# Performance work log

Hardware: AMD Instinct MI355X
Metric: run time of the kernel (lower is better)

## Reference

```python
import jax, jax.numpy as jnp
import numpy as np

N = 8192
NEG = -1e9  # masked-logit fill (finite to stay fp16/bf16-safe)


def _gat_layer(x, W, a_src, a_dst, adj, apply_elu):
    # x: [N, Fin], W: [Fin, Fout]
    h = x @ W                                   # [N, Fout]
    f_src = h @ a_src                           # [N] attention contribution of source i
    f_dst = h @ a_dst                           # [N] attention contribution of target j
    e = jax.nn.leaky_relu(f_src[:, None] + f_dst[None, :], negative_slope=0.2)  # [N, N]
    e = jnp.where(adj > 0, e, NEG)
    attn = jax.nn.softmax(e, axis=1)            # masked neighbor softmax per node
    out = attn @ h                              # [N, Fout]
    return jax.nn.elu(out) if apply_elu else out


def setup_inputs() -> dict:
    key = jax.random.key(0)
    ks = jax.random.split(key, 8)
    x = jax.random.normal(ks[0], (N, 512), dtype=jnp.float32)
    E_rand = 262144
    ei = jax.random.randint(ks[1], (2, E_rand), 0, N, dtype=jnp.int64)
    loops = jnp.broadcast_to(jnp.arange(N, dtype=jnp.int64), (2, N))
    edge_index = jnp.concatenate([ei, loops], axis=1)  # self-loops avoid empty softmax rows
    W1 = jax.random.normal(ks[2], (512, 256), dtype=jnp.float32) * (1.0 / np.sqrt(512))
    a1_src = jax.random.normal(ks[3], (256,), dtype=jnp.float32) * 0.1
    a1_dst = jax.random.normal(ks[4], (256,), dtype=jnp.float32) * 0.1
    W2 = jax.random.normal(ks[5], (256, 16), dtype=jnp.float32) * (1.0 / np.sqrt(256))
    a2_src = jax.random.normal(ks[6], (16,), dtype=jnp.float32) * 0.1
    a2_dst = jax.random.normal(ks[7], (16,), dtype=jnp.float32) * 0.1
    return {"x": x, "edge_index": edge_index, "W1": W1, "a1_src": a1_src,
            "a1_dst": a1_dst, "W2": W2, "a2_src": a2_src, "a2_dst": a2_dst}


def reference(x, edge_index, W1, a1_src, a1_dst, W2, a2_src, a2_dst):
    # dense adjacency scatter, exactly as the torch module does
    adj = jnp.zeros((N, N), dtype=x.dtype).at[edge_index[0], edge_index[1]].set(1.0)
    # inference: dropout disabled
    h = _gat_layer(x, W1, a1_src, a1_dst, adj, apply_elu=True)
    logits = _gat_layer(h, W2, a2_src, a2_dst, adj, apply_elu=False)
    return jax.nn.log_softmax(logits, axis=1)
```

## Files before the change

kernel.cpp:

```cpp
#include <hip/hip_runtime.h>
#include <hip/hip_bf16.h>


#define NN 8192
#define MAXD 128

typedef __bf16 bf16x8 __attribute__((ext_vector_type(8)));
typedef float f32x4 __attribute__((ext_vector_type(4)));
typedef unsigned short u16x8 __attribute__((ext_vector_type(8)));

__device__ __forceinline__ unsigned short f2bf(float f) {
  unsigned u = __float_as_uint(f);
  unsigned r = (u + 0x7fffu + ((u >> 16) & 1u)) >> 16;
  return (unsigned short)r;
}
__device__ __forceinline__ float bf2f(unsigned short u) {
  return __uint_as_float(((unsigned)u) << 16);
}
__device__ __forceinline__ float lrelu02(float e) { return e > 0.f ? e : 0.2f * e; }

__global__ __launch_bounds__(256) void prep_kernel(uint4* __restrict__ bitmap,
                                                   const float* __restrict__ W1,
                                                   unsigned short* __restrict__ W1t,
                                                   const float* __restrict__ W2,
                                                   unsigned short* __restrict__ W2t,
                                                   float4* __restrict__ f1sd) {
  const int bid = blockIdx.x, tid = threadIdx.x;
  if (bid < 2048) {
    bitmap[bid * 256 + tid] = uint4{0u, 0u, 0u, 0u};
  } else if (bid < 2560) {
    const int gid = (bid - 2048) * 256 + tid;
    const int n = gid >> 9, k = gid & 511;
    W1t[gid] = f2bf(W1[(size_t)k * 256 + n]);
  } else if (bid == 2560) {
    for (int i = tid; i < 16 * 256; i += 256) {
      const int n = i >> 8, k = i & 255;
      W2t[i] = f2bf(W2[(size_t)k * 16 + n]);
    }
  } else {
    for (int i = tid; i < 4096; i += 256) f1sd[i] = float4{0.f, 0.f, 0.f, 0.f};
  }
}

__global__ void scatter_kernel(const int* __restrict__ ei, int E,
                               unsigned* __restrict__ bitmap) {
  const int t = blockIdx.x * 256 + threadIdx.x;
  if (t >= E) return;
  const int s = ei[t];
  const int d = ei[E + t];
  atomicOr(bitmap + (size_t)s * 256 + (d >> 5), 1u << (d & 31));
}

__global__ __launch_bounds__(256) void gemm1_mfma_kernel(
    const float* __restrict__ X, const unsigned short* __restrict__ W1t,
    unsigned short* __restrict__ h1b, const float* __restrict__ A1S,
    const float* __restrict__ A1D, float* __restrict__ f1s, float* __restrict__ f1d) {
  constexpr int K = 512;
  __shared__ __align__(16) unsigned short lds[1024 * 8];
  const int t = threadIdx.x;
  const int w = t >> 6, l = t & 63;
  const int lr = l & 15, lg = l >> 4;
  const int bm = blockIdx.x * 64, bn = blockIdx.y * 64;
  const int r8 = t >> 3, c8 = t & 7;

  f32x4 acc[4];
  const f32x4 fz = {0.f, 0.f, 0.f, 0.f};
#pragma unroll
  for (int cb = 0; cb < 4; ++cb) acc[cb] = fz;

  for (int k0 = 0; k0 < K; k0 += 64) {
    float4 xa[2][2];
#pragma unroll
    for (int p = 0; p < 2; ++p) {
      const float* s = X + (size_t)(bm + r8 + p * 32) * K + k0 + c8 * 8;
      xa[p][0] = *(const float4*)s;
      xa[p][1] = *(const float4*)(s + 4);
    }
    uint4 wb[2];
#pragma unroll
    for (int p = 0; p < 2; ++p)
      wb[p] = *(const uint4*)(W1t + (size_t)(bn + r8 + p * 32) * K + k0 + c8 * 8);
    __syncthreads();
#pragma unroll
    for (int p = 0; p < 2; ++p) {
      const int row = r8 + p * 32;
      const int u = ((row >> 4) << 7) + ((c8 >> 2) << 6) + ((c8 & 3) << 4) + ((row & 15) ^ c8);
      u16x8 v;
      v[0] = f2bf(xa[p][0].x); v[1] = f2bf(xa[p][0].y);
      v[2] = f2bf(xa[p][0].z); v[3] = f2bf(xa[p][0].w);
      v[4] = f2bf(xa[p][1].x); v[5] = f2bf(xa[p][1].y);
      v[6] = f2bf(xa[p][1].z); v[7] = f2bf(xa[p][1].w);
      *(u16x8*)(lds + u * 8) = v;
    }
#pragma unroll
    for (int p = 0; p < 2; ++p) {
      const int row = r8 + p * 32;
      const int u = 512 + ((row >> 4) << 7) + ((c8 >> 2) << 6) + ((c8 & 3) << 4) + ((row & 15) ^ c8);
      *(uint4*)(lds + u * 8) = wb[p];
    }
    __syncthreads();
#pragma unroll
    for (int ks = 0; ks < 2; ++ks) {
      const int xr = lr ^ (ks * 4 + lg);
      const bf16x8 a = *(const bf16x8*)(lds + ((w << 7) + (ks << 6) + (lg << 4) + xr) * 8);
      const bf16x8 b0 = *(const bf16x8*)(lds + (512 + (0 << 7) + (ks << 6) + (lg << 4) + xr) * 8);
      const bf16x8 b1 = *(const bf16x8*)(lds + (512 + (1 << 7) + (ks << 6) + (lg << 4) + xr) * 8);
      const bf16x8 b2 = *(const bf16x8*)(lds + (512 + (2 << 7) + (ks << 6) + (lg << 4) + xr) * 8);
      const bf16x8 b3 = *(const bf16x8*)(lds + (512 + (3 << 7) + (ks << 6) + (lg << 4) + xr) * 8);
      acc[0] = __builtin_amdgcn_mfma_f32_16x16x32_bf16(a, b0, acc[0], 0, 0, 0);
      acc[1] = __builtin_amdgcn_mfma_f32_16x16x32_bf16(a, b1, acc[1], 0, 0, 0);
      acc[2] = __builtin_amdgcn_mfma_f32_16x16x32_bf16(a, b2, acc[2], 0, 0, 0);
      acc[3] = __builtin_amdgcn_mfma_f32_16x16x32_bf16(a, b3, acc[3], 0, 0, 0);
    }
  }
#pragma unroll
  for (int cb = 0; cb < 4; ++cb)
#pragma unroll
    for (int q = 0; q < 4; ++q) {
      const int row = bm + w * 16 + lg * 4 + q;
      h1b[(size_t)row * 256 + bn + cb * 16 + lr] = f2bf(acc[cb][q]);
    }
  float a1sv[4], a1dv[4];
#pragma unroll
  for (int cb = 0; cb < 4; ++cb) {
    a1sv[cb] = A1S[bn + cb * 16 + lr];
    a1dv[cb] = A1D[bn + cb * 16 + lr];
  }
#pragma unroll
  for (int q = 0; q < 4; ++q) {
    float ps = 0.f, pd = 0.f;
#pragma unroll
    for (int cb = 0; cb < 4; ++cb) {
      ps = fmaf(acc[cb][q], a1sv[cb], ps);
      pd = fmaf(acc[cb][q], a1dv[cb], pd);
    }
#pragma unroll
    for (int off = 8; off; off >>= 1) {
      ps += __shfl_xor(ps, off, 16);
      pd += __shfl_xor(pd, off, 16);
    }
    if (lr == 0) {
      const int row = bm + w * 16 + lg * 4 + q;
      atomicAdd(f1s + row, ps);
      atomicAdd(f1d + row, pd);
    }
  }
}

__global__ __launch_bounds__(256) void attn1_kernel(unsigned* __restrict__ bitmap,
                                                    int* __restrict__ degarr,
                                                    const unsigned short* __restrict__ h1b,
                                                    const float* __restrict__ fs,
                                                    const float* __restrict__ fd,
                                                    unsigned short* __restrict__ out1b) {
  __shared__ float wsh[4][MAXD];
  __shared__ int jsh[4][MAXD];
  const int lane = threadIdx.x & 63;
  const int wv = threadIdx.x >> 6;
  const int row = blockIdx.x * 4 + wv;
  unsigned* brow = bitmap + (size_t)row * 256;
  const uint4 wq = *(const uint4*)(brow + lane * 4);
  const int cnt = __popc(wq.x) + __popc(wq.y) + __popc(wq.z) + __popc(wq.w);
  int inc = cnt;
#pragma unroll
  for (int d = 1; d < 64; d <<= 1) {
    const int t2 = __shfl_up(inc, d);
    if (lane >= d) inc += t2;
  }
  int off = inc - cnt;
  const int deg = __shfl(inc, 63);
  {
    const unsigned words[4] = {wq.x, wq.y, wq.z, wq.w};
    const int base_j = lane * 128;
#pragma unroll
    for (int q = 0; q < 4; ++q) {
      unsigned word = words[q];
      while (word) {
        const int b = __ffs(word) - 1;
        word &= word - 1;
        jsh[wv][off++] = base_j + q * 32 + b;
      }
    }
  }
  if (lane == 0) degarr[row] = deg;
  {
    unsigned short* nbp = (unsigned short*)brow;
    if (lane < deg) nbp[lane] = (unsigned short)jsh[wv][lane];
    if (lane + 64 < deg) nbp[lane + 64] = (unsigned short)jsh[wv][lane + 64];
  }
  const float fsr = fs[row];
  const int j0 = (lane < deg) ? jsh[wv][lane] : 0;
  const int j1 = (lane + 64 < deg) ? jsh[wv][lane + 64] : 0;
  const float e0 = (lane < deg) ? lrelu02(fsr + fd[j0]) : -1e30f;
  const float e1 = (lane + 64 < deg) ? lrelu02(fsr + fd[j1]) : -1e30f;
  float m = fmaxf(e0, e1);
#pragma unroll
  for (int off2 = 32; off2; off2 >>= 1) m = fmaxf(m, __shfl_xor(m, off2));
  const float w0 = (lane < deg) ? expf(e0 - m) : 0.f;
  const float w1 = (lane + 64 < deg) ? expf(e1 - m) : 0.f;
  float s = w0 + w1;
#pragma unroll
  for (int off2 = 32; off2; off2 >>= 1) s += __shfl_xor(s, off2);
  wsh[wv][lane] = w0;
  wsh[wv][lane + 64] = w1;
  const int half = lane >> 5, lh = lane & 31;
  float acc[8] = {0.f, 0.f, 0.f, 0.f, 0.f, 0.f, 0.f, 0.f};
  int t = 0;
  for (; t + 8 <= deg; t += 8) {
    const int ja = jsh[wv][t + half], jb = jsh[wv][t + 2 + half];
    const int jc = jsh[wv][t + 4 + half], jd = jsh[wv][t + 6 + half];
    const float Wa = wsh[wv][t + half], Wb = wsh[wv][t + 2 + half];
    const float Wc = wsh[wv][t + 4 + half], Wd = wsh[wv][t + 6 + half];
    const u16x8 va = *(const u16x8*)(h1b + (size_t)ja * 256 + lh * 8);
    const u16x8 vb = *(const u16x8*)(h1b + (size_t)jb * 256 + lh * 8);
    const u16x8 vc = *(const u16x8*)(h1b + (size_t)jc * 256 + lh * 8);
    const u16x8 vd = *(const u16x8*)(h1b + (size_t)jd * 256 + lh * 8);
#pragma unroll
    for (int e = 0; e < 8; ++e)
      acc[e] = fmaf(Wa, bf2f(va[e]),
               fmaf(Wb, bf2f(vb[e]), fmaf(Wc, bf2f(vc[e]), fmaf(Wd, bf2f(vd[e]), acc[e]))));
  }
  for (; t < deg; t += 2) {
    const int idx = t + half;
    const int jt = (idx < deg) ? jsh[wv][idx] : 0;
    const float Wt = (idx < deg) ? wsh[wv][idx] : 0.f;
    const u16x8 v = *(const u16x8*)(h1b + (size_t)jt * 256 + lh * 8);
#pragma unroll
    for (int e = 0; e < 8; ++e) acc[e] = fmaf(Wt, bf2f(v[e]), acc[e]);
  }
#pragma unroll
  for (int e = 0; e < 8; ++e) acc[e] += __shfl_xor(acc[e], 32);
  const float inv = 1.f / s;
  u16x8 o;
#pragma unroll
  for (int e = 0; e < 8; ++e) {
    float v = acc[e] * inv;
    v = v > 0.f ? v : expf(v) - 1.f;
    o[e] = f2bf(v);
  }
  if (lane < 32) *(u16x8*)(out1b + (size_t)row * 256 + lh * 8) = o;
}

__global__ __launch_bounds__(256) void gemm2f2_kernel(
    const unsigned short* __restrict__ out1b, const unsigned short* __restrict__ W2t,
    const float* __restrict__ a2s, const float* __restrict__ a2d,
    float* __restrict__ h2, float* __restrict__ fs, float* __restrict__ fd) {
  const int l = threadIdx.x & 63, w = threadIdx.x >> 6;
  const int row0 = blockIdx.x * 64 + w * 16;
  const int lr = l & 15, lg = l >> 4;
  f32x4 acc = {0.f, 0.f, 0.f, 0.f};
#pragma unroll
  for (int k0 = 0; k0 < 256; k0 += 32) {
    const bf16x8 a = *(const bf16x8*)(out1b + (size_t)(row0 + lr) * 256 + k0 + lg * 8);
    const bf16x8 b = *(const bf16x8*)(W2t + (size_t)lr * 256 + k0 + lg * 8);
    acc = __builtin_amdgcn_mfma_f32_16x16x32_bf16(a, b, acc, 0, 0, 0);
  }
  const float as = a2s[lr], ad = a2d[lr];
#pragma unroll
  for (int q = 0; q < 4; ++q) {
    const int row = row0 + lg * 4 + q;
    const float v = acc[q];
    h2[(size_t)row * 16 + lr] = v;
    float ss = v * as, dd = v * ad;
#pragma unroll
    for (int off = 8; off; off >>= 1) {
      ss += __shfl_xor(ss, off, 16);
      dd += __shfl_xor(dd, off, 16);
    }
    if (lr == 0) {
      fs[row] = ss;
      fd[row] = dd;
    }
  }
}

__global__ __launch_bounds__(256) void attn2_kernel(const unsigned* __restrict__ bitmap,
                                                    const int* __restrict__ degarr,
                                                    const float* __restrict__ h2,
                                                    const float* __restrict__ fs,
                                                    const float* __restrict__ fd,
                                                    float* __restrict__ out) {
  __shared__ float wsh[4][MAXD];
  __shared__ int jsh[4][MAXD];
  const int lane = threadIdx.x & 63;
  const int wv = threadIdx.x >> 6;
  const int row = blockIdx.x * 4 + wv;
  const unsigned short* nb = (const unsigned short*)(bitmap + (size_t)row * 256);
  const int deg = degarr[row];
  const float fsr = fs[row];
  const int j0 = (lane < deg) ? (int)nb[lane] : 0;
  const int j1 = (lane + 64 < deg) ? (int)nb[lane + 64] : 0;
  const float e0 = (lane < deg) ? lrelu02(fsr + fd[j0]) : -1e30f;
  const float e1 = (lane + 64 < deg) ? lrelu02(fsr + fd[j1]) : -1e30f;
  float m = fmaxf(e0, e1);
#pragma unroll
  for (int off = 32; off; off >>= 1) m = fmaxf(m, __shfl_xor(m, off));
  const float w0 = (lane < deg) ? expf(e0 - m) : 0.f;
  const float w1 = (lane + 64 < deg) ? expf(e1 - m) : 0.f;
  float s = w0 + w1;
#pragma unroll
  for (int off = 32; off; off >>= 1) s += __shfl_xor(s, off);
  wsh[wv][lane] = w0;
  jsh[wv][lane] = j0;
  wsh[wv][lane + 64] = w1;
  jsh[wv][lane + 64] = j1;
  const int c = lane & 15, g = lane >> 4;
  float acc = 0.f;
  int t = g;
  for (; t + 12 < deg; t += 16) {
    const float W0 = wsh[wv][t], W1 = wsh[wv][t + 4];
    const float W2 = wsh[wv][t + 8], W3 = wsh[wv][t + 12];
    const float v0 = h2[(size_t)jsh[wv][t] * 16 + c];
    const float v1 = h2[(size_t)jsh[wv][t + 4] * 16 + c];
    const float v2 = h2[(size_t)jsh[wv][t + 8] * 16 + c];
    const float v3 = h2[(size_t)jsh[wv][t + 12] * 16 + c];
    acc = fmaf(W0, v0, fmaf(W1, v1, fmaf(W2, v2, fmaf(W3, v3, acc))));
  }
  for (; t < deg; t += 4) acc = fmaf(wsh[wv][t], h2[(size_t)jsh[wv][t] * 16 + c], acc);
  acc += __shfl_xor(acc, 16);
  acc += __shfl_xor(acc, 32);
  const float v = acc / s;
  float mx = v;
#pragma unroll
  for (int off = 8; off; off >>= 1) mx = fmaxf(mx, __shfl_xor(mx, off, 16));
  float se = expf(v - mx);
#pragma unroll
  for (int off = 8; off; off >>= 1) se += __shfl_xor(se, off, 16);
  if (lane < 16) out[(size_t)row * 16 + lane] = v - mx - logf(se);
}

extern "C" void kernel_launch(void* const* d_in, const int* in_sizes, int n_in,
                              void* d_out, int out_size, void* d_ws, size_t ws_size,
                              hipStream_t stream) {
  const float* x = (const float*)d_in[0];
  const int* ei = (const int*)d_in[1];
  const float* W1 = (const float*)d_in[2];
  const float* a1s = (const float*)d_in[3];
  const float* a1d = (const float*)d_in[4];
  const float* W2 = (const float*)d_in[5];
  const float* a2s = (const float*)d_in[6];
  const float* a2d = (const float*)d_in[7];
  float* out = (float*)d_out;
  const int E = in_sizes[1] / 2;

  char* ws = (char*)d_ws;
  unsigned short* h1b = (unsigned short*)ws;
  unsigned short* out1b = (unsigned short*)(ws + (4u << 20));
  unsigned* bitmap = (unsigned*)(ws + (16u << 20));
  float* f1s = (float*)(ws + (24u << 20));
  float* f1d = f1s + NN;
  float* h2 = f1d + NN;
  float* f2s = h2 + (size_t)NN * 16;
  float* f2d = f2s + NN;
  int* deg = (int*)(f2d + NN);
  unsigned short* w1t = (unsigned short*)(deg + NN);
  unsigned short* w2t = w1t + (size_t)256 * 512;

  prep_kernel<<<2562, 256, 0, stream>>>((uint4*)bitmap, W1, w1t, W2, w2t, (float4*)f1s);
  scatter_kernel<<<(E + 255) / 256, 256, 0, stream>>>(ei, E, bitmap);
  gemm1_mfma_kernel<<<dim3(NN / 64, 256 / 64), 256, 0, stream>>>(x, w1t, h1b, a1s, a1d,
                                                                 f1s, f1d);
  attn1_kernel<<<NN / 4, 256, 0, stream>>>(bitmap, deg, h1b, f1s, f1d, out1b);
  gemm2f2_kernel<<<NN / 64, 256, 0, stream>>>(out1b, w2t, a2s, a2d, h2, f2s, f2d);
  attn2_kernel<<<NN / 4, 256, 0, stream>>>(bitmap, deg, h2, f2s, f2d, out);
}
```

Measured before the change: 67.77 us.

## Fuse layer-2 projection and attention scores into attn1 epilogue

The attn1 kernel now keeps each row's ELU output in shared memory as fp32 and computes the 256x16 projection with W2 plus the layer-2 source/destination scores directly, removing the separate MFMA gemm2 kernel. This drops one kernel launch and the bf16 out1 round trip through global memory. In exchange, each wave does the small dot products with scalar FMAs and reads W2t per row, and the intermediate stays fp32 rather than being rounded to bf16.

```diff
diff --git a/kernel.cpp b/kernel.cpp
--- a/kernel.cpp
+++ b/kernel.cpp
@@ -152,9 +152,15 @@
                                                     const unsigned short* __restrict__ h1b,
                                                     const float* __restrict__ fs,
                                                     const float* __restrict__ fd,
-                                                    unsigned short* __restrict__ out1b) {
+                                                    const unsigned short* __restrict__ W2t,
+                                                    const float* __restrict__ a2s,
+                                                    const float* __restrict__ a2d,
+                                                    float* __restrict__ h2,
+                                                    float* __restrict__ f2s,
+                                                    float* __restrict__ f2d) {
   __shared__ float wsh[4][MAXD];
   __shared__ int jsh[4][MAXD];
+  __shared__ __align__(16) float orow[4][256];
   const int lane = threadIdx.x & 63;
   const int wv = threadIdx.x >> 6;
   const int row = blockIdx.x * 4 + wv;
@@ -231,46 +237,47 @@
 #pragma unroll
   for (int e = 0; e < 8; ++e) acc[e] += __shfl_xor(acc[e], 32);
   const float inv = 1.f / s;
-  u16x8 o;
+  float ve[8];
 #pragma unroll
   for (int e = 0; e < 8; ++e) {
     float v = acc[e] * inv;
-    v = v > 0.f ? v : expf(v) - 1.f;
-    o[e] = f2bf(v);
-  }
-  if (lane < 32) *(u16x8*)(out1b + (size_t)row * 256 + lh * 8) = o;
-}
-
-__global__ __launch_bounds__(256) void gemm2f2_kernel(
-    const unsigned short* __restrict__ out1b, const unsigned short* __restrict__ W2t,
-    const float* __restrict__ a2s, const float* __restrict__ a2d,
-    float* __restrict__ h2, float* __restrict__ fs, float* __restrict__ fd) {
-  const int l = threadIdx.x & 63, w = threadIdx.x >> 6;
-  const int row0 = blockIdx.x * 64 + w * 16;
-  const int lr = l & 15, lg = l >> 4;
-  f32x4 acc = {0.f, 0.f, 0.f, 0.f};
-#pragma unroll
-  for (int k0 = 0; k0 < 256; k0 += 32) {
-    const bf16x8 a = *(const bf16x8*)(out1b + (size_t)(row0 + lr) * 256 + k0 + lg * 8);
-    const bf16x8 b = *(const bf16x8*)(W2t + (size_t)lr * 256 + k0 + lg * 8);
-    acc = __builtin_amdgcn_mfma_f32_16x16x32_bf16(a, b, acc, 0, 0, 0);
-  }
-  const float as = a2s[lr], ad = a2d[lr];
-#pragma unroll
-  for (int q = 0; q < 4; ++q) {
-    const int row = row0 + lg * 4 + q;
-    const float v = acc[q];
-    h2[(size_t)row * 16 + lr] = v;
-    float ss = v * as, dd = v * ad;
-#pragma unroll
-    for (int off = 8; off; off >>= 1) {
-      ss += __shfl_xor(ss, off, 16);
-      dd += __shfl_xor(dd, off, 16);
-    }
-    if (lr == 0) {
-      fs[row] = ss;
-      fd[row] = dd;
-    }
+    ve[e] = v > 0.f ? v : expf(v) - 1.f;
+  }
+  if (lane < 32) {
+    const float4 o0 = {ve[0], ve[1], ve[2], ve[3]};
+    const float4 o1 = {ve[4], ve[5], ve[6], ve[7]};
+    *(float4*)&orow[wv][lh * 8] = o0;
+    *(float4*)&orow[wv][lh * 8 + 4] = o1;
+  }
+  const int c = lane & 15, g = lane >> 4;
+  float hsum = 0.f;
+#pragma unroll
+  for (int kb = 0; kb < 8; ++kb) {
+    const int kk = g * 64 + (((kb + g) & 7) << 3);
+    const float4 o0 = *(const float4*)&orow[wv][kk];
+    const float4 o1 = *(const float4*)&orow[wv][kk + 4];
+    const u16x8 w8 = *(const u16x8*)(W2t + (size_t)c * 256 + kk);
+    hsum = fmaf(o0.x, bf2f(w8[0]), hsum);
+    hsum = fmaf(o0.y, bf2f(w8[1]), hsum);
+    hsum = fmaf(o0.z, bf2f(w8[2]), hsum);
+    hsum = fmaf(o0.w, bf2f(w8[3]), hsum);
+    hsum = fmaf(o1.x, bf2f(w8[4]), hsum);
+    hsum = fmaf(o1.y, bf2f(w8[5]), hsum);
+    hsum = fmaf(o1.z, bf2f(w8[6]), hsum);
+    hsum = fmaf(o1.w, bf2f(w8[7]), hsum);
+  }
+  hsum += __shfl_xor(hsum, 16);
+  hsum += __shfl_xor(hsum, 32);
+  if (lane < 16) h2[(size_t)row * 16 + c] = hsum;
+  float ss = hsum * a2s[c], dd = hsum * a2d[c];
+#pragma unroll
+  for (int off2 = 8; off2; off2 >>= 1) {
+    ss += __shfl_xor(ss, off2, 16);
+    dd += __shfl_xor(dd, off2, 16);
+  }
+  if (lane == 0) {
+    f2s[row] = ss;
+    f2d[row] = dd;
   }
 }
 
@@ -345,7 +352,6 @@
 
   char* ws = (char*)d_ws;
   unsigned short* h1b = (unsigned short*)ws;
-  unsigned short* out1b = (unsigned short*)(ws + (4u << 20));
   unsigned* bitmap = (unsigned*)(ws + (16u << 20));
   float* f1s = (float*)(ws + (24u << 20));
   float* f1d = f1s + NN;
@@ -360,7 +366,7 @@
   scatter_kernel<<<(E + 255) / 256, 256, 0, stream>>>(ei, E, bitmap);
   gemm1_mfma_kernel<<<dim3(NN / 64, 256 / 64), 256, 0, stream>>>(x, w1t, h1b, a1s, a1d,
                                                                  f1s, f1d);
-  attn1_kernel<<<NN / 4, 256, 0, stream>>>(bitmap, deg, h1b, f1s, f1d, out1b);
-  gemm2f2_kernel<<<NN / 64, 256, 0, stream>>>(out1b, w2t, a2s, a2d, h2, f2s, f2d);
+  attn1_kernel<<<NN / 4, 256, 0, stream>>>(bitmap, deg, h1b, f1s, f1d, w2t, a2s, a2d,
+                                           h2, f2s, f2d);
   attn2_kernel<<<NN / 4, 256, 0, stream>>>(bitmap, deg, h2, f2s, f2d, out);
 }
```

After: 67.78 us. About the same (+0.0%).
